# Kernel optimization log

Measured on AMD Instinct MI355X. Metric: run time of the kernel, lower is better.

The kernel has to match this reference:

```python
import jax, jax.numpy as jnp
import numpy as np

NUM_CLASSES = 1000
EMBED_DIM = 256
N = 131072
MOMENTUM = 0.995
EPS = 1e-12  # F.normalize default eps


def _l2norm(x):
    # F.normalize: x / max(||x||_2, eps)
    n = jnp.sqrt(jnp.sum(x * x, axis=-1, keepdims=True))
    return x / jnp.maximum(n, EPS)


def setup_inputs() -> dict:
    key = jax.random.key(0)
    k1, k2, k3, k4 = jax.random.split(key, 4)
    z = jax.random.normal(k1, (N, EMBED_DIM), dtype=jnp.float32)
    prototypes = _l2norm(jax.random.normal(k2, (NUM_CLASSES, EMBED_DIM), dtype=jnp.float32))
    initialized = jax.random.randint(k3, (NUM_CLASSES,), 0, 2) > 0
    labels = jax.random.randint(k4, (N,), 0, NUM_CLASSES)
    return {"z": z, "prototypes": prototypes, "initialized": initialized, "labels": labels}


def reference(z, prototypes, initialized, labels):
    # Fused segment-mean-by-label + EMA-normalize update (ema_update).
    sums = jax.ops.segment_sum(z, labels, num_segments=NUM_CLASSES)          # [C, D]
    counts = jax.ops.segment_sum(jnp.ones((z.shape[0],), z.dtype), labels,
                                 num_segments=NUM_CLASSES)                    # [C]
    present = counts > 0                                                      # [C]
    mean_z = sums / jnp.maximum(counts, 1.0)[:, None]                         # [C, D]
    mean_n = _l2norm(mean_z)
    ema = _l2norm(MOMENTUM * prototypes + (1.0 - MOMENTUM) * mean_n)
    cand = jnp.where(initialized[:, None], ema, mean_n)
    new_protos = jnp.where(present[:, None], cand, prototypes)
    return new_protos
```

## Files before the change

kernel.cpp:

```cpp
#include <hip/hip_runtime.h>
#include <math.h>

static constexpr int   kC      = 1000;
static constexpr int   kStripe = 1024;
static constexpr int   kD      = 256;
static constexpr int   kCap    = 1024;
static constexpr int   kCntS   = 16;
static constexpr float kMom    = 0.995f;
static constexpr float kEps    = 1e-12f;

typedef float f32x4 __attribute__((ext_vector_type(4)));

__device__ __forceinline__ f32x4 nt_load4(const float* p) {
    return __builtin_nontemporal_load((const f32x4*)p);
}

__device__ __forceinline__ float block_sum256(float v) {
    __shared__ float lds[4];
    #pragma unroll
    for (int off = 32; off > 0; off >>= 1) v += __shfl_down(v, off, 64);
    __syncthreads();
    if ((threadIdx.x & 63) == 0) lds[threadIdx.x >> 6] = v;
    __syncthreads();
    return lds[0] + lds[1] + lds[2] + lds[3];
}

__global__ void __launch_bounds__(256)
k_scatter2(const int* __restrict__ labels, int n,
           unsigned short* __restrict__ cntmat,
           int* __restrict__ idx) {
    __shared__ unsigned int hcnt[kC];
    const int b   = blockIdx.x;
    const int tid = threadIdx.x;

    for (int c = tid; c < kC; c += 256) hcnt[c] = 0;
    __syncthreads();

    const int base = b * kStripe;
    const int m = min(kStripe, n - base);
    const size_t sbase = (size_t)b * kC * kStripe;

    if (m == kStripe) {
        const int4 l4 = ((const int4*)(labels + base))[tid];
        #pragma unroll
        for (int k = 0; k < 4; ++k) {
            const int lab = (&l4.x)[k];
            const unsigned int p = atomicAdd(&hcnt[lab], 1u);
            idx[sbase + (size_t)lab * kStripe + p] = base + tid * 4 + k;
        }
    } else {
        for (int j = tid; j < m; j += 256) {
            const int lab = labels[base + j];
            const unsigned int p = atomicAdd(&hcnt[lab], 1u);
            idx[sbase + (size_t)lab * kStripe + p] = base + j;
        }
    }
    __syncthreads();
    for (int c = tid; c < kC; c += 256)
        cntmat[(size_t)b * kC + c] = (unsigned short)hcnt[c];
}

__global__ void __launch_bounds__(256, 4)
k_reduce2(const float* __restrict__ z, const float* __restrict__ protos,
          const int* __restrict__ initialized,
          const unsigned short* __restrict__ cntmat, int B,
          const int* __restrict__ idx, float* __restrict__ out) {
    __shared__ int          sh_idx[kStripe];
    __shared__ float        sh_part[4][kD];
    __shared__ unsigned int s_pfx[256];

    const int c    = blockIdx.x;
    const int tid  = threadIdx.x;
    const int wave = tid >> 6;
    const int lane = tid & 63;

    const unsigned int myc = (tid < B) ? cntmat[(size_t)tid * kC + c] : 0u;

    s_pfx[tid] = myc;
    __syncthreads();
    for (int off = 1; off < 256; off <<= 1) {
        const unsigned int add = (tid >= off) ? s_pfx[tid - off] : 0u;
        __syncthreads();
        s_pfx[tid] += add;
        __syncthreads();
    }
    const unsigned int T  = s_pfx[255];
    const unsigned int ex = s_pfx[tid] - myc;

    f32x4 acc0 = {0.f, 0.f, 0.f, 0.f};
    f32x4 acc1 = {0.f, 0.f, 0.f, 0.f};

    for (unsigned int cb = 0; cb < T; cb += kStripe) {
        __syncthreads();
        if (myc > 0) {
            const size_t sb = ((size_t)tid * kC + c) * kStripe;
            for (unsigned int q = 0; q < myc; ++q) {
                const unsigned int g = ex + q;
                if (g >= cb && g < cb + kStripe) sh_idx[g - cb] = idx[sb + q];
            }
        }
        __syncthreads();

        const int mm = (int)min((unsigned int)kStripe, T - cb);
        int r = wave;
        for (; r + 28 < mm; r += 32) {
            const int i0 = sh_idx[r +  0]; const int i1 = sh_idx[r +  4];
            const int i2 = sh_idx[r +  8]; const int i3 = sh_idx[r + 12];
            const int i4 = sh_idx[r + 16]; const int i5 = sh_idx[r + 20];
            const int i6 = sh_idx[r + 24]; const int i7 = sh_idx[r + 28];
            const f32x4 a0 = nt_load4(z + (size_t)i0 * kD + lane * 4);
            const f32x4 a1 = nt_load4(z + (size_t)i1 * kD + lane * 4);
            const f32x4 a2 = nt_load4(z + (size_t)i2 * kD + lane * 4);
            const f32x4 a3 = nt_load4(z + (size_t)i3 * kD + lane * 4);
            const f32x4 a4 = nt_load4(z + (size_t)i4 * kD + lane * 4);
            const f32x4 a5 = nt_load4(z + (size_t)i5 * kD + lane * 4);
            const f32x4 a6 = nt_load4(z + (size_t)i6 * kD + lane * 4);
            const f32x4 a7 = nt_load4(z + (size_t)i7 * kD + lane * 4);
            acc0 += a0 + a1;
            acc1 += a2 + a3;
            acc0 += a4 + a5;
            acc1 += a6 + a7;
        }
        for (; r < mm; r += 4) {
            acc0 += nt_load4(z + (size_t)sh_idx[r] * kD + lane * 4);
        }
    }
    acc0 += acc1;

    __syncthreads();
    ((f32x4*)&sh_part[wave][lane * 4])[0] = acc0;
    __syncthreads();

    const int d = tid;
    const float sum = sh_part[0][d] + sh_part[1][d] + sh_part[2][d] + sh_part[3][d];
    const int cntc = (int)T;

    const float mean   = sum / fmaxf((float)cntc, 1.0f);
    const float nrm    = sqrtf(block_sum256(mean * mean));
    const float mean_n = mean / fmaxf(nrm, kEps);

    const float p    = protos[c * kD + d];
    const float e    = kMom * p + (1.0f - kMom) * mean_n;
    const float nrm2 = sqrtf(block_sum256(e * e));
    const float ema  = e / fmaxf(nrm2, kEps);

    const float cand = (initialized[c] != 0) ? ema : mean_n;
    __builtin_nontemporal_store((cntc > 0) ? cand : p, &out[c * kD + d]);
}

__global__ void k_scatter(const int* __restrict__ labels, int n,
                          int* __restrict__ cnt ,
                          int* __restrict__ idx,
                          int* __restrict__ ovf) {
    const int t = blockIdx.x * 256 + threadIdx.x;
    const int i0 = t * 4;
    if (i0 >= n) return;
    const int lim = min(4, n - i0);
    for (int k = 0; k < lim; ++k) {
        const int i = i0 + k;
        const int lab = labels[i];
        const int p = atomicAdd(&cnt[lab * kCntS], 1);
        if (p < kCap) {
            idx[(size_t)lab * kCap + p] = i;
        } else {
            const int q = atomicAdd(&ovf[0], 1);
            ovf[1 + 2 * q] = lab; ovf[2 + 2 * q] = i;
        }
    }
}

__global__ void __launch_bounds__(256, 4)
k_reduce(const float* __restrict__ z, const float* __restrict__ protos,
         const int* __restrict__ initialized, const int* __restrict__ cnt,
         const int* __restrict__ idx, const int* __restrict__ ovf,
         float* __restrict__ out) {
    __shared__ int   sh_idx[kCap];
    __shared__ float sh_part[4][kD];

    const int c    = blockIdx.x;
    const int tid  = threadIdx.x;
    const int wave = tid >> 6;
    const int lane = tid & 63;

    const int cntc = cnt[c * kCntS];
    const int m    = min(cntc, kCap);
    const int* __restrict__ cidx = idx + (size_t)c * kCap;

    for (int j = tid; j < m; j += 256) sh_idx[j] = cidx[j];
    __syncthreads();

    f32x4 acc0 = {0.f, 0.f, 0.f, 0.f};
    f32x4 acc1 = {0.f, 0.f, 0.f, 0.f};
    int r = wave;
    for (; r + 28 < m; r += 32) {
        const int i0 = sh_idx[r +  0]; const int i1 = sh_idx[r +  4];
        const int i2 = sh_idx[r +  8]; const int i3 = sh_idx[r + 12];
        const int i4 = sh_idx[r + 16]; const int i5 = sh_idx[r + 20];
        const int i6 = sh_idx[r + 24]; const int i7 = sh_idx[r + 28];
        const f32x4 a0 = nt_load4(z + (size_t)i0 * kD + lane * 4);
        const f32x4 a1 = nt_load4(z + (size_t)i1 * kD + lane * 4);
        const f32x4 a2 = nt_load4(z + (size_t)i2 * kD + lane * 4);
        const f32x4 a3 = nt_load4(z + (size_t)i3 * kD + lane * 4);
        const f32x4 a4 = nt_load4(z + (size_t)i4 * kD + lane * 4);
        const f32x4 a5 = nt_load4(z + (size_t)i5 * kD + lane * 4);
        const f32x4 a6 = nt_load4(z + (size_t)i6 * kD + lane * 4);
        const f32x4 a7 = nt_load4(z + (size_t)i7 * kD + lane * 4);
        acc0 += a0 + a1; acc1 += a2 + a3;
        acc0 += a4 + a5; acc1 += a6 + a7;
    }
    for (; r < m; r += 4) acc0 += nt_load4(z + (size_t)sh_idx[r] * kD + lane * 4);
    acc0 += acc1;

    ((f32x4*)&sh_part[wave][lane * 4])[0] = acc0;
    __syncthreads();

    const int d = tid;
    float sum = sh_part[0][d] + sh_part[1][d] + sh_part[2][d] + sh_part[3][d];
    const int novf = ovf[0];
    if (novf > 0) {
        for (int j = 0; j < novf; ++j)
            if (ovf[1 + 2 * j] == c) sum += z[(size_t)ovf[2 + 2 * j] * kD + d];
    }

    const float mean   = sum / fmaxf((float)cntc, 1.0f);
    const float nrm    = sqrtf(block_sum256(mean * mean));
    const float mean_n = mean / fmaxf(nrm, kEps);
    const float p    = protos[c * kD + d];
    const float e    = kMom * p + (1.0f - kMom) * mean_n;
    const float nrm2 = sqrtf(block_sum256(e * e));
    const float ema  = e / fmaxf(nrm2, kEps);
    const float cand = (initialized[c] != 0) ? ema : mean_n;
    __builtin_nontemporal_store((cntc > 0) ? cand : p, &out[c * kD + d]);
}

extern "C" void kernel_launch(void* const* d_in, const int* in_sizes, int n_in,
                              void* d_out, int out_size, void* d_ws, size_t ws_size,
                              hipStream_t stream) {
    const float* z           = (const float*)d_in[0];
    const float* protos      = (const float*)d_in[1];
    const int*   initialized = (const int*)d_in[2];
    const int*   labels      = (const int*)d_in[3];
    const int n = in_sizes[3];
    float* out = (float*)d_out;

    const int B = (n + kStripe - 1) / kStripe;
    const size_t cnt_bytes = (((size_t)B * kC * sizeof(unsigned short)) + 255) & ~(size_t)255;
    const size_t need2 = cnt_bytes + (size_t)B * kC * kStripe * sizeof(int);

    if (B <= 256 && ws_size >= need2) {
        unsigned short* cntmat = (unsigned short*)d_ws;
        int* idx = (int*)((char*)d_ws + cnt_bytes);
        k_scatter2<<<B, 256, 0, stream>>>(labels, n, cntmat, idx);
        k_reduce2 <<<kC, 256, 0, stream>>>(z, protos, initialized, cntmat, B,
                                           idx, out);
        return;
    }

    int* ws  = (int*)d_ws;
    int* cnt = ws;
    int* ovf = ws + 1024 * kCntS;
    int* idx = ws + 1024 * kCntS + 8 + 2 * n;
    (void)hipMemsetAsync(ws, 0, (size_t)(1024 * kCntS + 8) * sizeof(int), stream);
    const int threads = (n + 3) / 4;
    const int blocks = (threads + 255) / 256;
    k_scatter<<<blocks, 256, 0, stream>>>(labels, n, cnt, idx, ovf);
    k_reduce <<<kC, 256, 0, stream>>>(z, protos, initialized, cnt, idx, ovf, out);
}
```

Baseline: 37.60 us.

## Use 16-bit stripe-local indices, smaller stripes, and a wave-shuffle prefix scan

Halves the stripe size to 512 so each scatter block covers fewer labels, giving more scatter blocks, and stores per-class indices as 16-bit offsets local to the stripe. The global row is rebuilt in the reduce kernel from the stripe number. The 256-entry LDS Hillis-Steele prefix scan, with its many barriers, is replaced by a wave-level shuffle scan plus a 4-entry cross-wave combine. It also drops the occupancy hint from launch bounds and adds a 16-row unrolled tail in the gather loop. The aim is to cut workspace index traffic and scan sync overhead, at the cost of a tighter B<=256 limit on the fast path.

```diff
diff --git a/kernel.cpp b/kernel.cpp
--- a/kernel.cpp
+++ b/kernel.cpp
@@ -2,7 +2,7 @@
 #include <math.h>
 
 static constexpr int   kC      = 1000;
-static constexpr int   kStripe = 1024;
+static constexpr int   kStripe = 512;
 static constexpr int   kD      = 256;
 static constexpr int   kCap    = 1024;
 static constexpr int   kCntS   = 16;
@@ -28,7 +28,7 @@
 __global__ void __launch_bounds__(256)
 k_scatter2(const int* __restrict__ labels, int n,
            unsigned short* __restrict__ cntmat,
-           int* __restrict__ idx) {
+           unsigned short* __restrict__ idx16) {
     __shared__ unsigned int hcnt[kC];
     const int b   = blockIdx.x;
     const int tid = threadIdx.x;
@@ -41,18 +41,19 @@
     const size_t sbase = (size_t)b * kC * kStripe;
 
     if (m == kStripe) {
-        const int4 l4 = ((const int4*)(labels + base))[tid];
+        const int2 l2 = ((const int2*)(labels + base))[tid];
         #pragma unroll
-        for (int k = 0; k < 4; ++k) {
-            const int lab = (&l4.x)[k];
+        for (int k = 0; k < 2; ++k) {
+            const int lab = (&l2.x)[k];
             const unsigned int p = atomicAdd(&hcnt[lab], 1u);
-            idx[sbase + (size_t)lab * kStripe + p] = base + tid * 4 + k;
+            idx16[sbase + (size_t)lab * kStripe + p] =
+                (unsigned short)(tid * 2 + k);
         }
     } else {
         for (int j = tid; j < m; j += 256) {
             const int lab = labels[base + j];
             const unsigned int p = atomicAdd(&hcnt[lab], 1u);
-            idx[sbase + (size_t)lab * kStripe + p] = base + j;
+            idx16[sbase + (size_t)lab * kStripe + p] = (unsigned short)j;
         }
     }
     __syncthreads();
@@ -60,14 +61,14 @@
         cntmat[(size_t)b * kC + c] = (unsigned short)hcnt[c];
 }
 
-__global__ void __launch_bounds__(256, 4)
+__global__ void __launch_bounds__(256)
 k_reduce2(const float* __restrict__ z, const float* __restrict__ protos,
           const int* __restrict__ initialized,
           const unsigned short* __restrict__ cntmat, int B,
-          const int* __restrict__ idx, float* __restrict__ out) {
-    __shared__ int          sh_idx[kStripe];
+          const unsigned short* __restrict__ idx16, float* __restrict__ out) {
+    __shared__ int          sh_idx[1024];
     __shared__ float        sh_part[4][kD];
-    __shared__ unsigned int s_pfx[256];
+    __shared__ unsigned int wtot[4];
 
     const int c    = blockIdx.x;
     const int tid  = threadIdx.x;
@@ -76,32 +77,37 @@
 
     const unsigned int myc = (tid < B) ? cntmat[(size_t)tid * kC + c] : 0u;
 
-    s_pfx[tid] = myc;
-    __syncthreads();
-    for (int off = 1; off < 256; off <<= 1) {
-        const unsigned int add = (tid >= off) ? s_pfx[tid - off] : 0u;
-        __syncthreads();
-        s_pfx[tid] += add;
-        __syncthreads();
-    }
-    const unsigned int T  = s_pfx[255];
-    const unsigned int ex = s_pfx[tid] - myc;
+    unsigned int s = myc;
+    #pragma unroll
+    for (int off = 1; off < 64; off <<= 1) {
+        const unsigned int t = __shfl_up(s, off, 64);
+        if (lane >= off) s += t;
+    }
+    if (lane == 63) wtot[wave] = s;
+    __syncthreads();
+    unsigned int wbase = 0;
+    #pragma unroll
+    for (int w = 0; w < 4; ++w) wbase += (w < wave) ? wtot[w] : 0u;
+    const unsigned int T  = wtot[0] + wtot[1] + wtot[2] + wtot[3];
+    const unsigned int ex = wbase + s - myc;
 
     f32x4 acc0 = {0.f, 0.f, 0.f, 0.f};
     f32x4 acc1 = {0.f, 0.f, 0.f, 0.f};
 
-    for (unsigned int cb = 0; cb < T; cb += kStripe) {
+    for (unsigned int cb = 0; cb < T; cb += 1024) {
         __syncthreads();
         if (myc > 0) {
             const size_t sb = ((size_t)tid * kC + c) * kStripe;
+            const int rowbase = tid * kStripe;
             for (unsigned int q = 0; q < myc; ++q) {
                 const unsigned int g = ex + q;
-                if (g >= cb && g < cb + kStripe) sh_idx[g - cb] = idx[sb + q];
+                if (g >= cb && g < cb + 1024)
+                    sh_idx[g - cb] = rowbase + (int)idx16[sb + q];
             }
         }
         __syncthreads();
 
-        const int mm = (int)min((unsigned int)kStripe, T - cb);
+        const int mm = (int)min(1024u, T - cb);
         int r = wave;
         for (; r + 28 < mm; r += 32) {
             const int i0 = sh_idx[r +  0]; const int i1 = sh_idx[r +  4];
@@ -121,6 +127,16 @@
             acc0 += a4 + a5;
             acc1 += a6 + a7;
         }
+        for (; r + 12 < mm; r += 16) {
+            const int i0 = sh_idx[r +  0]; const int i1 = sh_idx[r +  4];
+            const int i2 = sh_idx[r +  8]; const int i3 = sh_idx[r + 12];
+            const f32x4 a0 = nt_load4(z + (size_t)i0 * kD + lane * 4);
+            const f32x4 a1 = nt_load4(z + (size_t)i1 * kD + lane * 4);
+            const f32x4 a2 = nt_load4(z + (size_t)i2 * kD + lane * 4);
+            const f32x4 a3 = nt_load4(z + (size_t)i3 * kD + lane * 4);
+            acc0 += a0 + a1;
+            acc1 += a2 + a3;
+        }
         for (; r < mm; r += 4) {
             acc0 += nt_load4(z + (size_t)sh_idx[r] * kD + lane * 4);
         }
@@ -244,15 +260,17 @@
     float* out = (float*)d_out;
 
     const int B = (n + kStripe - 1) / kStripe;
-    const size_t cnt_bytes = (((size_t)B * kC * sizeof(unsigned short)) + 255) & ~(size_t)255;
-    const size_t need2 = cnt_bytes + (size_t)B * kC * kStripe * sizeof(int);
+    const size_t cnt_bytes = (((size_t)B * kC * sizeof(unsigned short)) + 255)
+                             & ~(size_t)255;
+    const size_t need2 = cnt_bytes
+                       + (size_t)B * kC * kStripe * sizeof(unsigned short);
 
     if (B <= 256 && ws_size >= need2) {
         unsigned short* cntmat = (unsigned short*)d_ws;
-        int* idx = (int*)((char*)d_ws + cnt_bytes);
-        k_scatter2<<<B, 256, 0, stream>>>(labels, n, cntmat, idx);
+        unsigned short* idx16  = (unsigned short*)((char*)d_ws + cnt_bytes);
+        k_scatter2<<<B, 256, 0, stream>>>(labels, n, cntmat, idx16);
         k_reduce2 <<<kC, 256, 0, stream>>>(z, protos, initialized, cntmat, B,
-                                           idx, out);
+                                           idx16, out);
         return;
     }
 
```

Measured after the change: 36.99 us. No clear change (-1.6%).
